# Kernel tuning notes

Measured on AMD Instinct MI355X. Metric: run time of the kernel, lower is better.

The kernel has to match this reference:

```python
import jax, jax.numpy as jnp
import numpy as np

N_NODES = 100000
N_EDGES = 1600000
H_FEATS = 128


def setup_inputs() -> dict:
    key = jax.random.key(0)
    ks = jax.random.split(key, 9)
    h = jax.random.normal(ks[0], (N_NODES, H_FEATS), dtype=jnp.float32)
    src_idx = jax.random.randint(ks[1], (N_EDGES,), 0, N_NODES, dtype=jnp.int64)
    dst_idx = jax.random.randint(ks[2], (N_EDGES,), 0, N_NODES, dtype=jnp.int64)
    # nn.Linear weights: [out, in], kaiming-uniform-ish init approximated with scaled normal
    W1 = jax.random.normal(ks[3], (H_FEATS, 2 * H_FEATS), dtype=jnp.float32) * (1.0 / np.sqrt(2 * H_FEATS))
    b1 = jax.random.normal(ks[4], (H_FEATS,), dtype=jnp.float32) * 0.01
    W2 = jax.random.normal(ks[5], (H_FEATS, H_FEATS), dtype=jnp.float32) * (1.0 / np.sqrt(H_FEATS))
    b2 = jax.random.normal(ks[6], (H_FEATS,), dtype=jnp.float32) * 0.01
    W3 = jax.random.normal(ks[7], (1, H_FEATS), dtype=jnp.float32) * (1.0 / np.sqrt(H_FEATS))
    b3 = jax.random.normal(ks[8], (1,), dtype=jnp.float32) * 0.01
    return {"h": h, "src_idx": src_idx, "dst_idx": dst_idx,
            "W1": W1, "b1": b1, "W2": W2, "b2": b2, "W3": W3, "b3": b3}


def reference(h, src_idx, dst_idx, W1, b1, W2, b2, W3, b3):
    # Gather src/dst node features per edge and concat: [E, 2*h_feats]
    he = jnp.concatenate([h[src_idx], h[dst_idx]], axis=1)
    # 3-layer MLP: Linear -> ReLU -> Linear -> ReLU -> Linear -> squeeze
    x = jax.nn.relu(he @ W1.T + b1)
    x = jax.nn.relu(x @ W2.T + b2)
    score = (x @ W3.T + b3)[:, 0]  # [E]
    return score
```

## Files before the change

### kernel.cpp

```cpp
#include <hip/hip_runtime.h>
#include <hip/hip_fp16.h>

typedef _Float16 f16;
typedef __attribute__((ext_vector_type(8))) _Float16 f16x8;
typedef __attribute__((ext_vector_type(4))) _Float16 f16x4;
typedef __attribute__((ext_vector_type(2))) __fp16 fp16x2;
typedef __attribute__((ext_vector_type(4))) float f32x4;

__global__ void cvt_h_f16(const float* __restrict__ h, f16* __restrict__ hf, int n4) {
    int stride = gridDim.x * blockDim.x;
    for (int i = blockIdx.x * blockDim.x + threadIdx.x; i < n4; i += stride) {
        float4 v = reinterpret_cast<const float4*>(h)[i];
        f16x4 o = { (f16)v.x, (f16)v.y, (f16)v.z, (f16)v.w };
        reinterpret_cast<f16x4*>(hf)[i] = o;
    }
}

__global__ __launch_bounds__(256, 2)
void build_uv(const float* __restrict__ h, const float* __restrict__ W1,
              const float* __restrict__ b1,
              f16* __restrict__ U, f16* __restrict__ V, int nNodes)
{
    __shared__ f16 hS[64 * 128];
    __shared__ f16 xS[64 * 128];

    const int tid = threadIdx.x;
    const int w = tid >> 6, l = tid & 63, g = l >> 4, c = l & 15;

    f16x8 waf[4][2], wbf[4][2];
    f32x4 b1v[2];
    #pragma unroll
    for (int nt = 0; nt < 2; ++nt) {
        const int n = w * 32 + nt * 16 + c;
        #pragma unroll
        for (int ks = 0; ks < 4; ++ks) {
            const float4* pa = reinterpret_cast<const float4*>(W1 + n * 256 + ks * 32 + g * 8);
            const float4* pb = reinterpret_cast<const float4*>(W1 + n * 256 + 128 + ks * 32 + g * 8);
            float4 a0 = pa[0], a1 = pa[1], b0 = pb[0], b1_ = pb[1];
            f16x8 va = { (f16)a0.x,(f16)a0.y,(f16)a0.z,(f16)a0.w,
                         (f16)a1.x,(f16)a1.y,(f16)a1.z,(f16)a1.w };
            f16x8 vb = { (f16)b0.x,(f16)b0.y,(f16)b0.z,(f16)b0.w,
                         (f16)b1_.x,(f16)b1_.y,(f16)b1_.z,(f16)b1_.w };
            waf[ks][nt] = va;
            wbf[ks][nt] = vb;
        }
        b1v[nt] = *reinterpret_cast<const f32x4*>(b1 + w * 32 + nt * 16 + g * 4);
    }

    const int node0 = blockIdx.x * 64;
    {
        const int m = tid >> 2, q4 = tid & 3;
        const int node = node0 + m;
        if (node < nNodes) {
            const float4* src = reinterpret_cast<const float4*>(h + (size_t)node * 128) + q4 * 8;
            #pragma unroll
            for (int j = 0; j < 4; ++j) {
                float4 a = src[2 * j], b = src[2 * j + 1];
                f16x8 v = { (f16)a.x,(f16)a.y,(f16)a.z,(f16)a.w,
                            (f16)b.x,(f16)b.y,(f16)b.z,(f16)b.w };
                const int chs = (q4 * 4 + j) ^ (m & 7);
                *reinterpret_cast<f16x8*>(&hS[m * 128 + chs * 8]) = v;
            }
        } else {
            #pragma unroll
            for (int j = 0; j < 4; ++j) {
                const int chs = (q4 * 4 + j) ^ (m & 7);
                *reinterpret_cast<f16x8*>(&hS[m * 128 + chs * 8]) = (f16x8)(f16)0;
            }
        }
    }
    __syncthreads();

    f32x4 acc[4][2];
    #pragma unroll
    for (int et = 0; et < 4; ++et) { acc[et][0] = (f32x4){0,0,0,0}; acc[et][1] = (f32x4){0,0,0,0}; }
    #pragma unroll
    for (int ks = 0; ks < 4; ++ks) {
        #pragma unroll
        for (int et = 0; et < 4; ++et) {
            const int row = et * 16 + c;
            const int chs = (ks * 4 + g) ^ (row & 7);
            f16x8 hb = *reinterpret_cast<const f16x8*>(&hS[row * 128 + chs * 8]);
            acc[et][0] = __builtin_amdgcn_mfma_f32_16x16x32_f16(waf[ks][0], hb, acc[et][0], 0, 0, 0);
            acc[et][1] = __builtin_amdgcn_mfma_f32_16x16x32_f16(waf[ks][1], hb, acc[et][1], 0, 0, 0);
        }
    }
    #pragma unroll
    for (int et = 0; et < 4; ++et) {
        #pragma unroll
        for (int nt = 0; nt < 2; ++nt) {
            f32x4 v = acc[et][nt] + b1v[nt];
            f16x4 p = { (f16)v[0], (f16)v[1], (f16)v[2], (f16)v[3] };
            const int row = et * 16 + c;
            const int n0 = w * 32 + nt * 16 + g * 4;
            const int chs = (n0 >> 3) ^ (row & 7);
            *reinterpret_cast<f16x4*>(&xS[row * 128 + chs * 8 + (n0 & 7)]) = p;
        }
    }
    __syncthreads();
    {
        const int m = tid >> 2, q4 = tid & 3;
        const int node = node0 + m;
        if (node < nNodes) {
            #pragma unroll
            for (int j = 0; j < 4; ++j) {
                const int lc = q4 * 4 + j;
                const int chs = lc ^ (m & 7);
                uint4 val = *reinterpret_cast<const uint4*>(&xS[m * 128 + chs * 8]);
                reinterpret_cast<uint4*>(U + (size_t)node * 128)[lc] = val;
            }
        }
    }
    __syncthreads();

    #pragma unroll
    for (int et = 0; et < 4; ++et) { acc[et][0] = (f32x4){0,0,0,0}; acc[et][1] = (f32x4){0,0,0,0}; }
    #pragma unroll
    for (int ks = 0; ks < 4; ++ks) {
        #pragma unroll
        for (int et = 0; et < 4; ++et) {
            const int row = et * 16 + c;
            const int chs = (ks * 4 + g) ^ (row & 7);
            f16x8 hb = *reinterpret_cast<const f16x8*>(&hS[row * 128 + chs * 8]);
            acc[et][0] = __builtin_amdgcn_mfma_f32_16x16x32_f16(wbf[ks][0], hb, acc[et][0], 0, 0, 0);
            acc[et][1] = __builtin_amdgcn_mfma_f32_16x16x32_f16(wbf[ks][1], hb, acc[et][1], 0, 0, 0);
        }
    }
    #pragma unroll
    for (int et = 0; et < 4; ++et) {
        #pragma unroll
        for (int nt = 0; nt < 2; ++nt) {
            f32x4 v = acc[et][nt];
            f16x4 p = { (f16)v[0], (f16)v[1], (f16)v[2], (f16)v[3] };
            const int row = et * 16 + c;
            const int n0 = w * 32 + nt * 16 + g * 4;
            const int chs = (n0 >> 3) ^ (row & 7);
            *reinterpret_cast<f16x4*>(&xS[row * 128 + chs * 8 + (n0 & 7)]) = p;
        }
    }
    __syncthreads();
    {
        const int m = tid >> 2, q4 = tid & 3;
        const int node = node0 + m;
        if (node < nNodes) {
            #pragma unroll
            for (int j = 0; j < 4; ++j) {
                const int lc = q4 * 4 + j;
                const int chs = lc ^ (m & 7);
                uint4 val = *reinterpret_cast<const uint4*>(&xS[m * 128 + chs * 8]);
                reinterpret_cast<uint4*>(V + (size_t)node * 128)[lc] = val;
            }
        }
    }
}

__global__ __launch_bounds__(256, 4)
void mlp_edges_uv(const f16* __restrict__ U, const f16* __restrict__ V,
                  const int* __restrict__ srcI, const int* __restrict__ dstI,
                  const float* __restrict__ W2, const float* __restrict__ b2,
                  const float* __restrict__ W3, const float* __restrict__ b3,
                  float* __restrict__ out, int E, int ntiles)
{
    __shared__ f16 uS[64 * 128];
    __shared__ f16 vS[64 * 128];
    __shared__ float sbuf[4][64];

    const int tid = threadIdx.x;
    const int w = tid >> 6, l = tid & 63, g = l >> 4, c = l & 15;
    const int grid = gridDim.x;

    f16x8 w2f[4][2];
    f32x4 b2v[2], w3v[2];
    #pragma unroll
    for (int nt = 0; nt < 2; ++nt) {
        const int n = w * 32 + nt * 16 + c;
        #pragma unroll
        for (int ks = 0; ks < 4; ++ks) {
            const float4* p = reinterpret_cast<const float4*>(W2 + n * 128 + ks * 32 + g * 8);
            float4 a = p[0], b = p[1];
            f16x8 v = { (f16)a.x,(f16)a.y,(f16)a.z,(f16)a.w,
                        (f16)b.x,(f16)b.y,(f16)b.z,(f16)b.w };
            w2f[ks][nt] = v;
        }
        const int base = w * 32 + nt * 16 + g * 4;
        b2v[nt] = *reinterpret_cast<const f32x4*>(b2 + base);
        w3v[nt] = *reinterpret_cast<const f32x4*>(W3 + base);
    }
    const float b3s = b3[0];

    const int p_ = tid >> 1, q_ = tid & 1;
    const int m_ = p_ & 63;
    const int hh = p_ >> 6;
    const int* __restrict__ idxArr = hh ? dstI : srcI;
    const f16* __restrict__ tab = hh ? V : U;
    f16* dstS = hh ? vS : uS;

    auto loadIdx = [&](int t) -> int {
        int e = t * 64 + m_;
        return (e < E) ? idxArr[e] : 0;
    };
    auto stage = [&](int node) {
        const uint4* src = reinterpret_cast<const uint4*>(tab + (size_t)node * 128) + q_ * 8;
        #pragma unroll
        for (int j = 0; j < 8; ++j) {
            uint4 v = src[j];
            const int chs = (q_ * 8 + j) ^ (m_ & 7);
            *reinterpret_cast<uint4*>(&dstS[m_ * 128 + chs * 8]) = v;
        }
    };

    const int t0 = blockIdx.x;
    int nIdx = (t0 < ntiles) ? loadIdx(t0) : 0;

    for (int t = t0; t < ntiles; t += grid) {
        stage(nIdx);
        __syncthreads();
        nIdx = (t + grid < ntiles) ? loadIdx(t + grid) : 0;

        f32x4 acc[4][2];
        #pragma unroll
        for (int et = 0; et < 4; ++et) { acc[et][0] = (f32x4){0,0,0,0}; acc[et][1] = (f32x4){0,0,0,0}; }
        #pragma unroll
        for (int ks = 0; ks < 4; ++ks) {
            #pragma unroll
            for (int et = 0; et < 4; ++et) {
                const int edge = et * 16 + c;
                const int chs = (ks * 4 + g) ^ (edge & 7);
                f16x8 uf = *reinterpret_cast<const f16x8*>(&uS[edge * 128 + chs * 8]);
                f16x8 vf = *reinterpret_cast<const f16x8*>(&vS[edge * 128 + chs * 8]);
                f16x8 xf = uf + vf;
                #pragma unroll
                for (int j = 0; j < 8; ++j) xf[j] = xf[j] > (f16)0 ? xf[j] : (f16)0;
                acc[et][0] = __builtin_amdgcn_mfma_f32_16x16x32_f16(w2f[ks][0], xf, acc[et][0], 0, 0, 0);
                acc[et][1] = __builtin_amdgcn_mfma_f32_16x16x32_f16(w2f[ks][1], xf, acc[et][1], 0, 0, 0);
            }
        }

        #pragma unroll
        for (int et = 0; et < 4; ++et) {
            f32x4 sv = {0.f,0.f,0.f,0.f};
            #pragma unroll
            for (int nt = 0; nt < 2; ++nt) {
                f32x4 v = acc[et][nt] + b2v[nt];
                #pragma unroll
                for (int r = 0; r < 4; ++r) {
                    float x = v[r] > 0.f ? v[r] : 0.f;
                    sv[r] += x * w3v[nt][r];
                }
            }
            float part = sv[0] + sv[1] + sv[2] + sv[3];
            part += __shfl_xor(part, 16, 64);
            part += __shfl_xor(part, 32, 64);
            if (g == 0) sbuf[w][et * 16 + c] = part;
        }
        __syncthreads();

        if (tid < 64) {
            const int e = t * 64 + tid;
            if (e < E)
                out[e] = sbuf[0][tid] + sbuf[1][tid] + sbuf[2][tid] + sbuf[3][tid] + b3s;
        }
    }
}

template<int USEF16>
__global__ __launch_bounds__(256, 3)
void mlp_edges(const float* __restrict__ h32, const f16* __restrict__ hf,
               const int* __restrict__ srcI, const int* __restrict__ dstI,
               const float* __restrict__ W1, const float* __restrict__ b1,
               const float* __restrict__ W2, const float* __restrict__ b2,
               const float* __restrict__ W3, const float* __restrict__ b3,
               float* __restrict__ out, int E, int ntiles)
{
    __shared__ f16 heS[64 * 256];
    __shared__ f16 x1S[64 * 128];
    __shared__ float sbuf[4][64];

    const int tid = threadIdx.x;
    const int w = tid >> 6, l = tid & 63, g = l >> 4, c = l & 15;
    const int grid = gridDim.x;

    f16x8 w1f[8][2], w2f[4][2];
    f32x4 b1v[2], b2v[2], w3v[2];
    #pragma unroll
    for (int nt = 0; nt < 2; ++nt) {
        const int n = w * 32 + nt * 16 + c;
        #pragma unroll
        for (int ks = 0; ks < 8; ++ks) {
            const float4* p = reinterpret_cast<const float4*>(W1 + n * 256 + ks * 32 + g * 8);
            float4 a = p[0], b = p[1];
            f16x8 v = { (f16)a.x,(f16)a.y,(f16)a.z,(f16)a.w,
                        (f16)b.x,(f16)b.y,(f16)b.z,(f16)b.w };
            w1f[ks][nt] = v;
        }
        #pragma unroll
        for (int ks = 0; ks < 4; ++ks) {
            const float4* p = reinterpret_cast<const float4*>(W2 + n * 128 + ks * 32 + g * 8);
            float4 a = p[0], b = p[1];
            f16x8 v = { (f16)a.x,(f16)a.y,(f16)a.z,(f16)a.w,
                        (f16)b.x,(f16)b.y,(f16)b.z,(f16)b.w };
            w2f[ks][nt] = v;
        }
        const int base = w * 32 + nt * 16 + g * 4;
        b1v[nt] = *reinterpret_cast<const f32x4*>(b1 + base);
        b2v[nt] = *reinterpret_cast<const f32x4*>(b2 + base);
        w3v[nt] = *reinterpret_cast<const f32x4*>(W3 + base);
    }
    const float b3s = b3[0];

    const int p_ = tid >> 1, q_ = tid & 1;
    const int m_ = p_ & 63;
    const int hh = p_ >> 6;
    const int* __restrict__ idxArr = hh ? dstI : srcI;

    auto loadIdx = [&](int t) -> int {
        int e = t * 64 + m_;
        return (e < E) ? idxArr[e] : 0;
    };
    auto stage = [&](int node) {
        if (USEF16) {
            const uint4* src = reinterpret_cast<const uint4*>(hf + (size_t)node * 128) + q_ * 8;
            #pragma unroll
            for (int j = 0; j < 8; ++j) {
                uint4 v = src[j];
                const int chs = (hh * 16 + q_ * 8 + j) ^ (m_ & 7);
                *reinterpret_cast<uint4*>(&heS[m_ * 256 + chs * 8]) = v;
            }
        } else {
            const float4* src = reinterpret_cast<const float4*>(h32 + (size_t)node * 128) + q_ * 16;
            #pragma unroll
            for (int j = 0; j < 8; ++j) {
                float4 a = src[2 * j], b = src[2 * j + 1];
                f16x8 v = { (f16)a.x,(f16)a.y,(f16)a.z,(f16)a.w,
                            (f16)b.x,(f16)b.y,(f16)b.z,(f16)b.w };
                const int chs = (hh * 16 + q_ * 8 + j) ^ (m_ & 7);
                *reinterpret_cast<f16x8*>(&heS[m_ * 256 + chs * 8]) = v;
            }
        }
    };

    const int t0 = blockIdx.x;
    int nIdx = (t0 < ntiles) ? loadIdx(t0) : 0;

    for (int t = t0; t < ntiles; t += grid) {
        stage(nIdx);
        __syncthreads();
        nIdx = (t + grid < ntiles) ? loadIdx(t + grid) : 0;

        f32x4 acc[4][2];
        #pragma unroll
        for (int et = 0; et < 4; ++et) { acc[et][0] = (f32x4){0,0,0,0}; acc[et][1] = (f32x4){0,0,0,0}; }
        #pragma unroll
        for (int ks = 0; ks < 8; ++ks) {
            #pragma unroll
            for (int et = 0; et < 4; ++et) {
                const int edge = et * 16 + c;
                const int chs = (ks * 4 + g) ^ (edge & 7);
                f16x8 hb = *reinterpret_cast<const f16x8*>(&heS[edge * 256 + chs * 8]);
                acc[et][0] = __builtin_amdgcn_mfma_f32_16x16x32_f16(w1f[ks][0], hb, acc[et][0], 0, 0, 0);
                acc[et][1] = __builtin_amdgcn_mfma_f32_16x16x32_f16(w1f[ks][1], hb, acc[et][1], 0, 0, 0);
            }
        }
        #pragma unroll
        for (int et = 0; et < 4; ++et) {
            #pragma unroll
            for (int nt = 0; nt < 2; ++nt) {
                f32x4 v = acc[et][nt] + b1v[nt];
                #pragma unroll
                for (int r = 0; r < 4; ++r) v[r] = v[r] > 0.f ? v[r] : 0.f;
                union { fp16x2 h2[2]; uint2 u; } uu;
                uu.h2[0] = __builtin_amdgcn_cvt_pkrtz(v[0], v[1]);
                uu.h2[1] = __builtin_amdgcn_cvt_pkrtz(v[2], v[3]);
                const int edge = et * 16 + c;
                const int n0 = w * 32 + nt * 16 + g * 4;
                const int chs = (n0 >> 3) ^ (edge & 7);
                *reinterpret_cast<uint2*>(&x1S[edge * 128 + chs * 8 + (n0 & 7)]) = uu.u;
            }
        }
        __syncthreads();

        #pragma unroll
        for (int et = 0; et < 4; ++et) { acc[et][0] = (f32x4){0,0,0,0}; acc[et][1] = (f32x4){0,0,0,0}; }
        #pragma unroll
        for (int ks = 0; ks < 4; ++ks) {
            #pragma unroll
            for (int et = 0; et < 4; ++et) {
                const int edge = et * 16 + c;
                const int chs = (ks * 4 + g) ^ (edge & 7);
                f16x8 xb = *reinterpret_cast<const f16x8*>(&x1S[edge * 128 + chs * 8]);
                acc[et][0] = __builtin_amdgcn_mfma_f32_16x16x32_f16(w2f[ks][0], xb, acc[et][0], 0, 0, 0);
                acc[et][1] = __builtin_amdgcn_mfma_f32_16x16x32_f16(w2f[ks][1], xb, acc[et][1], 0, 0, 0);
            }
        }
        #pragma unroll
        for (int et = 0; et < 4; ++et) {
            f32x4 sv = {0.f,0.f,0.f,0.f};
            #pragma unroll
            for (int nt = 0; nt < 2; ++nt) {
                f32x4 v = acc[et][nt] + b2v[nt];
                #pragma unroll
                for (int r = 0; r < 4; ++r) {
                    float x = v[r] > 0.f ? v[r] : 0.f;
                    sv[r] += x * w3v[nt][r];
                }
            }
            float part = sv[0] + sv[1] + sv[2] + sv[3];
            part += __shfl_xor(part, 16, 64);
            part += __shfl_xor(part, 32, 64);
            if (g == 0) sbuf[w][et * 16 + c] = part;
        }
        __syncthreads();

        if (tid < 64) {
            const int e = t * 64 + tid;
            if (e < E)
                out[e] = sbuf[0][tid] + sbuf[1][tid] + sbuf[2][tid] + sbuf[3][tid] + b3s;
        }
    }
}

extern "C" void kernel_launch(void* const* d_in, const int* in_sizes, int n_in,
                              void* d_out, int out_size, void* d_ws, size_t ws_size,
                              hipStream_t stream) {
    const float* h  = (const float*)d_in[0];
    const int* srcI = (const int*)d_in[1];
    const int* dstI = (const int*)d_in[2];
    const float* W1 = (const float*)d_in[3];
    const float* b1 = (const float*)d_in[4];
    const float* W2 = (const float*)d_in[5];
    const float* b2 = (const float*)d_in[6];
    const float* W3 = (const float*)d_in[7];
    const float* b3 = (const float*)d_in[8];
    float* out = (float*)d_out;

    const int E = in_sizes[1];
    const int hElems = in_sizes[0];
    const int nNodes = hElems / 128;
    const int ntiles = (E + 63) / 64;

    const size_t uvBytes = 2 * (size_t)nNodes * 128 * sizeof(f16);
    if (ws_size >= uvBytes) {
        f16* U = (f16*)d_ws;
        f16* V = U + (size_t)nNodes * 128;
        build_uv<<<(nNodes + 63) / 64, 256, 0, stream>>>(h, W1, b1, U, V, nNodes);
        const int grid = ntiles < 1024 ? ntiles : 1024;
        mlp_edges_uv<<<grid, 256, 0, stream>>>(U, V, srcI, dstI, W2, b2, W3, b3, out, E, ntiles);
    } else {
        f16* hf = (f16*)d_ws;
        const bool useF16 = (ws_size >= (size_t)hElems * sizeof(f16));
        if (useF16) cvt_h_f16<<<2048, 256, 0, stream>>>(h, hf, hElems / 4);
        const int grid = ntiles < 768 ? ntiles : 768;
        if (useF16)
            mlp_edges<1><<<grid, 256, 0, stream>>>(h, hf, srcI, dstI, W1, b1, W2, b2, W3, b3, out, E, ntiles);
        else
            mlp_edges<0><<<grid, 256, 0, stream>>>(h, hf, srcI, dstI, W1, b1, W2, b2, W3, b3, out, E, ntiles);
    }
}
```

Measured before the change: 182.0 us.

## Gather U/V rows directly into MFMA registers, drop LDS staging

The edge MLP kernel no longer stages the gathered U and V rows through shared memory. Each lane loads its own edge's src/dst indices and reads the fp16 rows straight from global memory into MFMA operand registers. The reduction buffer is double-buffered by tile parity, which removes one __syncthreads per tile. This cuts LDS traffic and a barrier, but each of the four waves now redundantly gathers the same 64 edges' rows and index prefetching is lost, which relies on the cache to absorb the duplicate reads.

```diff
diff --git a/kernel.cpp b/kernel.cpp
--- a/kernel.cpp
+++ b/kernel.cpp
@@ -155,15 +155,13 @@
 }
 
 __global__ __launch_bounds__(256, 4)
-void mlp_edges_uv(const f16* __restrict__ U, const f16* __restrict__ V,
-                  const int* __restrict__ srcI, const int* __restrict__ dstI,
-                  const float* __restrict__ W2, const float* __restrict__ b2,
-                  const float* __restrict__ W3, const float* __restrict__ b3,
-                  float* __restrict__ out, int E, int ntiles)
+void mlp_edges_uv2(const f16* __restrict__ U, const f16* __restrict__ V,
+                   const int* __restrict__ srcI, const int* __restrict__ dstI,
+                   const float* __restrict__ W2, const float* __restrict__ b2,
+                   const float* __restrict__ W3, const float* __restrict__ b3,
+                   float* __restrict__ out, int E, int ntiles)
 {
-    __shared__ f16 uS[64 * 128];
-    __shared__ f16 vS[64 * 128];
-    __shared__ float sbuf[4][64];
+    __shared__ float sbuf[2][4][64];
 
     const int tid = threadIdx.x;
     const int w = tid >> 6, l = tid & 63, g = l >> 4, c = l & 15;
@@ -188,47 +186,31 @@
     }
     const float b3s = b3[0];
 
-    const int p_ = tid >> 1, q_ = tid & 1;
-    const int m_ = p_ & 63;
-    const int hh = p_ >> 6;
-    const int* __restrict__ idxArr = hh ? dstI : srcI;
-    const f16* __restrict__ tab = hh ? V : U;
-    f16* dstS = hh ? vS : uS;
-
-    auto loadIdx = [&](int t) -> int {
-        int e = t * 64 + m_;
-        return (e < E) ? idxArr[e] : 0;
-    };
-    auto stage = [&](int node) {
-        const uint4* src = reinterpret_cast<const uint4*>(tab + (size_t)node * 128) + q_ * 8;
-        #pragma unroll
-        for (int j = 0; j < 8; ++j) {
-            uint4 v = src[j];
-            const int chs = (q_ * 8 + j) ^ (m_ & 7);
-            *reinterpret_cast<uint4*>(&dstS[m_ * 128 + chs * 8]) = v;
-        }
-    };
-
-    const int t0 = blockIdx.x;
-    int nIdx = (t0 < ntiles) ? loadIdx(t0) : 0;
-
-    for (int t = t0; t < ntiles; t += grid) {
-        stage(nIdx);
-        __syncthreads();
-        nIdx = (t + grid < ntiles) ? loadIdx(t + grid) : 0;
+    int par = 0;
+    for (int t = blockIdx.x; t < ntiles; t += grid, par ^= 1) {
+        const int e0 = t * 64;
 
         f32x4 acc[4][2];
         #pragma unroll
         for (int et = 0; et < 4; ++et) { acc[et][0] = (f32x4){0,0,0,0}; acc[et][1] = (f32x4){0,0,0,0}; }
-        #pragma unroll
-        for (int ks = 0; ks < 4; ++ks) {
-            #pragma unroll
-            for (int et = 0; et < 4; ++et) {
-                const int edge = et * 16 + c;
-                const int chs = (ks * 4 + g) ^ (edge & 7);
-                f16x8 uf = *reinterpret_cast<const f16x8*>(&uS[edge * 128 + chs * 8]);
-                f16x8 vf = *reinterpret_cast<const f16x8*>(&vS[edge * 128 + chs * 8]);
-                f16x8 xf = uf + vf;
+
+        #pragma unroll
+        for (int et = 0; et < 4; ++et) {
+            const int e = e0 + et * 16 + c;
+            const bool eok = (e < E);
+            const int si = eok ? srcI[e] : 0;
+            const int di = eok ? dstI[e] : 0;
+            const uint4* up = reinterpret_cast<const uint4*>(U + (size_t)si * 128);
+            const uint4* vp = reinterpret_cast<const uint4*>(V + (size_t)di * 128);
+            uint4 uf[4], vf[4];
+            #pragma unroll
+            for (int ks = 0; ks < 4; ++ks) {
+                uf[ks] = up[ks * 4 + g];
+                vf[ks] = vp[ks * 4 + g];
+            }
+            #pragma unroll
+            for (int ks = 0; ks < 4; ++ks) {
+                f16x8 xf = *reinterpret_cast<f16x8*>(&uf[ks]) + *reinterpret_cast<f16x8*>(&vf[ks]);
                 #pragma unroll
                 for (int j = 0; j < 8; ++j) xf[j] = xf[j] > (f16)0 ? xf[j] : (f16)0;
                 acc[et][0] = __builtin_amdgcn_mfma_f32_16x16x32_f16(w2f[ks][0], xf, acc[et][0], 0, 0, 0);
@@ -251,14 +233,15 @@
             float part = sv[0] + sv[1] + sv[2] + sv[3];
             part += __shfl_xor(part, 16, 64);
             part += __shfl_xor(part, 32, 64);
-            if (g == 0) sbuf[w][et * 16 + c] = part;
+            if (g == 0) sbuf[par][w][et * 16 + c] = part;
         }
         __syncthreads();
 
         if (tid < 64) {
-            const int e = t * 64 + tid;
+            const int e = e0 + tid;
             if (e < E)
-                out[e] = sbuf[0][tid] + sbuf[1][tid] + sbuf[2][tid] + sbuf[3][tid] + b3s;
+                out[e] = sbuf[par][0][tid] + sbuf[par][1][tid]
+                       + sbuf[par][2][tid] + sbuf[par][3][tid] + b3s;
         }
     }
 }
@@ -444,7 +427,7 @@
         f16* V = U + (size_t)nNodes * 128;
         build_uv<<<(nNodes + 63) / 64, 256, 0, stream>>>(h, W1, b1, U, V, nNodes);
         const int grid = ntiles < 1024 ? ntiles : 1024;
-        mlp_edges_uv<<<grid, 256, 0, stream>>>(U, V, srcI, dstI, W2, b2, W3, b3, out, E, ntiles);
+        mlp_edges_uv2<<<grid, 256, 0, stream>>>(U, V, srcI, dstI, W2, b2, W3, b3, out, E, ntiles);
     } else {
         f16* hf = (f16*)d_ws;
         const bool useF16 = (ws_size >= (size_t)hElems * sizeof(f16));
```

After: 433.4 us. 138% more time.
